# Kernel tuning notes

Hardware: AMD Instinct MI355X
Metric: run time of the kernel (lower is better)

## Reference

```python
import jax, jax.numpy as jnp
import numpy as np

EPS = 1e-12  # F.normalize eps
TEMP = 0.03


def _l2norm(x):
    # torch F.normalize: x / max(||x||, eps)
    n = jnp.sqrt(jnp.sum(x * x, axis=-1, keepdims=True))
    return x / jnp.maximum(n, EPS)


def setup_inputs() -> dict:
    key = jax.random.key(0)
    ks = jax.random.split(key, 8)
    B, C, H, W = 8, 256, 64, 64
    M = 2024
    Ch = C // 4
    s = 1.0 / np.sqrt(C)
    return {
        "feats": jax.random.normal(ks[0], (B, C, H, W), jnp.float32),
        "fg_memory": jax.random.normal(ks[1], (M, C), jnp.float32) * s,
        "bg_memory": jax.random.normal(ks[2], (M, C), jnp.float32) * s,
        "w1_fg": jax.random.normal(ks[3], (C, Ch), jnp.float32) * s,
        "b1_fg": jnp.zeros((Ch,), jnp.float32),
        "w2_fg": jax.random.normal(ks[4], (Ch, 1), jnp.float32) * (1.0 / np.sqrt(Ch)),
        "b2_fg": jnp.zeros((1,), jnp.float32),
        "w1_bg": jax.random.normal(ks[5], (C, Ch), jnp.float32) * s,
        "b1_bg": jnp.zeros((Ch,), jnp.float32),
        "w2_bg": jax.random.normal(ks[6], (Ch, 1), jnp.float32) * (1.0 / np.sqrt(Ch)),
        "b2_bg": jnp.zeros((1,), jnp.float32),
    }


def _gate(x, w1, b1, w2, b2):
    h = jax.nn.relu(x @ w1 + b1)
    return jax.nn.sigmoid(h @ w2 + b2)  # [N,1]


def reference(feats, fg_memory, bg_memory, w1_fg, b1_fg, w2_fg, b2_fg,
              w1_bg, b1_bg, w2_bg, b2_bg):
    B, C, H, W = feats.shape
    x = jnp.transpose(feats, (0, 2, 3, 1)).reshape(-1, C)  # [N,C]
    xn = _l2norm(x)
    fgn = _l2norm(fg_memory)  # [M,C]
    bgn = _l2norm(bg_memory)

    attn_fg = jax.nn.softmax((xn @ fgn.T) / TEMP, axis=1)  # [N,M]
    mem_fg = attn_fg @ fgn                                  # [N,C]
    attn_bg = jax.nn.softmax((xn @ bgn.T) / TEMP, axis=1)
    mem_bg = attn_bg @ bgn

    g_fg = _gate(xn, w1_fg, b1_fg, w2_fg, b2_fg)
    g_bg = _gate(xn, w1_bg, b1_bg, w2_bg, b2_bg)

    fused = xn + g_fg * mem_fg - g_bg * mem_bg
    return jnp.transpose(fused.reshape(B, H, W, C), (0, 3, 1, 2))
```

## Files before the change

kernel.cpp:

```cpp
#include <hip/hip_runtime.h>
#include <math.h>

#define B_   8
#define C_   256
#define HW_  4096
#define N_   32768
#define M_   2024
#define MP_  2048
#define CH_  64
#define NCHUNK (MP_ / 64)
#define INV_TEMP 33.333333333333336f
#define NEPS 1e-12f

typedef __attribute__((ext_vector_type(8))) short short8;
typedef __attribute__((ext_vector_type(4))) float floatx4;

__device__ __forceinline__ unsigned short f2bf(float f) {
  union { float f; unsigned u; } v; v.f = f;
  unsigned r = v.u + 0x7FFFu + ((v.u >> 16) & 1u);
  return (unsigned short)(r >> 16);
}
__device__ __forceinline__ float bf2f(unsigned short b) {
  union { unsigned u; float f; } v; v.u = ((unsigned)b) << 16; return v.f;
}

__device__ __forceinline__ void barrier_lds_only() {
  asm volatile("s_waitcnt lgkmcnt(0)\n\ts_barrier" ::: "memory");
}

__device__ __forceinline__ void async_copy16(const unsigned short* gsrc,
                                             unsigned short* lds) {
  __builtin_amdgcn_global_load_lds(
      (const __attribute__((address_space(1))) void*)gsrc,
      (__attribute__((address_space(3))) void*)lds, 16, 0, 0);
}

__global__ __launch_bounds__(256) void norm_mem_kernel(
    const float* __restrict__ fg, const float* __restrict__ bg,
    const float* __restrict__ w1f, const float* __restrict__ w1b,
    unsigned short* __restrict__ fgS, unsigned short* __restrict__ bgS,
    unsigned short* __restrict__ fgT, unsigned short* __restrict__ bgT) {
  __shared__ unsigned short tile[64][258];
  int bid = blockIdx.x;
  int t = threadIdx.x;
  int rr = t >> 2, c4 = t & 3;

  if (bid >= 64) {
    const float* srcw = (bid == 64) ? w1f : w1b;
    unsigned short* ms = (bid == 64) ? fgS : bgS;
#pragma unroll
    for (int i = 0; i < 16; ++i) {
      int c = c4 * 64 + i * 4;
      ushort4 o;
      o.x = f2bf(srcw[(size_t)(c + 0) * CH_ + rr]);
      o.y = f2bf(srcw[(size_t)(c + 1) * CH_ + rr]);
      o.z = f2bf(srcw[(size_t)(c + 2) * CH_ + rr]);
      o.w = f2bf(srcw[(size_t)(c + 3) * CH_ + rr]);
      int unit = (32 * 32 + (c >> 5) * 4 + ((c >> 3) & 3)) * 64 + rr;
      *(ushort4*)&ms[(size_t)unit * 8 + (c & 7)] = o;
    }
    return;
  }

  const float* src; unsigned short *ms, *mt; int r0;
  if (bid < 32) { src = fg; ms = fgS; mt = fgT; r0 = bid * 64; }
  else          { src = bg; ms = bgS; mt = bgT; r0 = (bid - 32) * 64; }
  int row = r0 + rr;
  int chunk = r0 >> 6;
  float v[64];
  float s = 0.f;
  if (row < M_) {
    const float4* p = (const float4*)(src + (size_t)row * C_ + c4 * 64);
#pragma unroll
    for (int i = 0; i < 16; ++i) {
      float4 q = p[i];
      v[i * 4 + 0] = q.x; v[i * 4 + 1] = q.y; v[i * 4 + 2] = q.z; v[i * 4 + 3] = q.w;
      s += q.x * q.x + q.y * q.y + q.z * q.z + q.w * q.w;
    }
  } else {
#pragma unroll
    for (int i = 0; i < 64; ++i) v[i] = 0.f;
  }
  s += __shfl_xor(s, 1, 64);
  s += __shfl_xor(s, 2, 64);
  float inv = (row < M_) ? 1.0f / fmaxf(sqrtf(s), NEPS) : 0.f;
#pragma unroll
  for (int i = 0; i < 16; ++i) {
    int c = c4 * 64 + i * 4;
    ushort4 o;
    o.x = f2bf(v[i * 4 + 0] * inv); o.y = f2bf(v[i * 4 + 1] * inv);
    o.z = f2bf(v[i * 4 + 2] * inv); o.w = f2bf(v[i * 4 + 3] * inv);
    int unit = (chunk * 32 + (c >> 5) * 4 + ((c >> 3) & 3)) * 64 + rr;
    *(ushort4*)&ms[(size_t)unit * 8 + (c & 7)] = o;
    *(ushort4*)&tile[rr][c] = o;
  }
  __syncthreads();
  int m = t & 63, cw = t >> 6;
#pragma unroll 8
  for (int j = 0; j < 64; ++j) {
    int c = cw * 64 + j;
    mt[(size_t)c * MP_ + r0 + m] = tile[m][c];
  }
}

__global__ __launch_bounds__(256) void prep_x_kernel(
    const float* __restrict__ feats, float* __restrict__ invn,
    unsigned short* __restrict__ xnb) {
  __shared__ unsigned short tileb[256][66];
  __shared__ float part[4][64];
  __shared__ float invs[64];
  int t = threadIdx.x, hwl = t & 63, cw = t >> 6;
  int n0 = blockIdx.x * 64;
  int b = n0 >> 12, hw0 = n0 & 4095;
  const float* p = feats + (size_t)b * C_ * HW_ + hw0 + hwl;
  float s = 0.f;
#pragma unroll 8
  for (int i = 0; i < 64; ++i) {
    int c = cw * 64 + i;
    float v = p[(size_t)c * HW_];
    s += v * v;
    tileb[c][hwl] = f2bf(v);
  }
  part[cw][hwl] = s;
  __syncthreads();
  if (t < 64) {
    float tot = part[0][t] + part[1][t] + part[2][t] + part[3][t];
    float inv = 1.0f / fmaxf(sqrtf(tot), NEPS);
    invn[n0 + t] = inv;
    invs[t] = inv;
  }
  __syncthreads();
  int px = t >> 2, q = t & 3;
  float iv = invs[px];
  unsigned short* xp = xnb + (size_t)(n0 + px) * C_;
#pragma unroll
  for (int blk = 0; blk < 8; ++blk) {
    int cb = blk * 4 + q;
    short8 o;
#pragma unroll
    for (int j = 0; j < 8; ++j)
      o[j] = (short)f2bf(bf2f(tileb[cb * 8 + j][px]) * iv);
    *(short8*)&xp[cb * 8] = o;
  }
}

__device__ __forceinline__ void stage_chunk(const unsigned short* memS, int mc,
                                            unsigned short* mtile, int w, int l) {
  const unsigned short* src = memS + (size_t)mc * 16384;
#pragma unroll
  for (int it = 0; it < 4; ++it) {
    int seg = (it * 8 + w) * 512;
    async_copy16(src + seg + l * 8, mtile + seg);
  }
}

__global__ __launch_bounds__(512, 4) void flash_fused_kernel(
    const unsigned short* __restrict__ xnb,
    const unsigned short* __restrict__ fgS, const unsigned short* __restrict__ fgT,
    const unsigned short* __restrict__ bgS, const unsigned short* __restrict__ bgT,
    const float* __restrict__ feats, const float* __restrict__ invn,
    const float* __restrict__ b1fp, const float* __restrict__ w2fp,
    const float* __restrict__ b2fp, const float* __restrict__ b1bp,
    const float* __restrict__ w2bp, const float* __restrict__ b2bp,
    float* __restrict__ out) {
  __shared__ __align__(16) char smem[49920];
  unsigned short* mtile = (unsigned short*)smem;
  unsigned short* Pbuf0 = (unsigned short*)(smem + 32768);
  unsigned short* Pbuf1 = (unsigned short*)(smem + 40960);
  float* rowsum = (float*)(smem + 49152);
  float* comb   = (float*)(smem + 49408);
  float* gpart  = (float*)(smem + 49664);
  float* trans  = (float*)smem;

  int t = threadIdx.x;
  int w = t >> 6, l = t & 63;
  int lm = l & 15, quad = l >> 4;
  int rg = w & 3, mh = w >> 2;
  int row0 = blockIdx.x * 64;

  short8 afrag[8];
  {
    const unsigned short* ap = xnb + (size_t)(row0 + 16 * rg + lm) * C_ + quad * 8;
#pragma unroll
    for (int kb = 0; kb < 8; ++kb)
      afrag[kb] = *(const short8*)(ap + kb * 32);
  }

  int bb = row0 >> 12, hw0 = row0 & 4095;
  float iv = invn[row0 + l];
  size_t ob = (size_t)bb * (size_t)C_ * HW_ + hw0 + l;

#pragma unroll 1
  for (int pass = 0; pass < 2; ++pass) {
    const unsigned short* memS  = pass ? bgS : fgS;
    const unsigned short* membT = pass ? bgT : fgT;

    floatx4 accO[4][2];
#pragma unroll
    for (int rt = 0; rt < 4; ++rt)
#pragma unroll
      for (int ct = 0; ct < 2; ++ct) accO[rt][ct] = (floatx4){0.f, 0.f, 0.f, 0.f};
    float rs[4] = {0.f, 0.f, 0.f, 0.f};
    if (t < 64) { rowsum[t] = 0.f; gpart[t] = 0.f; }

    stage_chunk(memS, 0, mtile, w, l);

#pragma unroll 1
    for (int mc = 0; mc < NCHUNK; ++mc) {
      __syncthreads();

      short8 bfT[2][2];
#pragma unroll
      for (int ct = 0; ct < 2; ++ct) {
        const unsigned short* tp =
            membT + (size_t)(w * 32 + ct * 16 + lm) * MP_ + mc * 64 + quad * 8;
        bfT[ct][0] = *(const short8*)(tp);
        bfT[ct][1] = *(const short8*)(tp + 32);
      }

      floatx4 accS[2];
      accS[0] = (floatx4){0.f, 0.f, 0.f, 0.f};
      accS[1] = (floatx4){0.f, 0.f, 0.f, 0.f};
#pragma unroll
      for (int mt2 = 0; mt2 < 2; ++mt2) {
        int mrow = mh * 32 + mt2 * 16 + lm;
#pragma unroll
        for (int kb = 0; kb < 8; ++kb) {
          short8 bf = *(const short8*)&mtile[(size_t)(((kb * 4 + quad) * 64) + mrow) * 8];
          accS[mt2] = __builtin_amdgcn_mfma_f32_16x16x32_bf16(afrag[kb], bf, accS[mt2], 0, 0, 0);
        }
      }

      unsigned short* P = (mc & 1) ? Pbuf1 : Pbuf0;
#pragma unroll
      for (int mt2 = 0; mt2 < 2; ++mt2) {
        int m = mh * 32 + mt2 * 16 + lm;
        float ebias = (mc * 64 + m < M_) ? 0.f : -1e30f;
        int g = mh * 4 + mt2 * 2 + (lm >> 3);
#pragma unroll
        for (int r = 0; r < 4; ++r) {
          float pv = __expf(__builtin_fmaf(accS[mt2][r], INV_TEMP, ebias));
          unsigned short pb = f2bf(pv);
          rs[r] += bf2f(pb);
          P[(g * 64 + 16 * rg + quad * 4 + r) * 8 + (lm & 7)] = pb;
        }
      }
      barrier_lds_only();

      stage_chunk(memS, mc + 1, mtile, w, l);

#pragma unroll
      for (int rt = 0; rt < 4; ++rt) {
        short8 pf0 = *(const short8*)&P[(size_t)((0 + quad) * 64 + rt * 16 + lm) * 8];
        short8 pf1 = *(const short8*)&P[(size_t)((4 + quad) * 64 + rt * 16 + lm) * 8];
#pragma unroll
        for (int ct = 0; ct < 2; ++ct) {
          accO[rt][ct] = __builtin_amdgcn_mfma_f32_16x16x32_bf16(pf0, bfT[ct][0], accO[rt][ct], 0, 0, 0);
          accO[rt][ct] = __builtin_amdgcn_mfma_f32_16x16x32_bf16(pf1, bfT[ct][1], accO[rt][ct], 0, 0, 0);
        }
      }
    }

    __syncthreads();
    {
      const float* b1p = pass ? b1bp : b1fp;
      const float* w2p = pass ? w2bp : w2fp;
      floatx4 accS[2];
      accS[0] = (floatx4){0.f, 0.f, 0.f, 0.f};
      accS[1] = (floatx4){0.f, 0.f, 0.f, 0.f};
#pragma unroll
      for (int mt2 = 0; mt2 < 2; ++mt2) {
        int mrow = mh * 32 + mt2 * 16 + lm;
#pragma unroll
        for (int kb = 0; kb < 8; ++kb) {
          short8 bf = *(const short8*)&mtile[(size_t)(((kb * 4 + quad) * 64) + mrow) * 8];
          accS[mt2] = __builtin_amdgcn_mfma_f32_16x16x32_bf16(afrag[kb], bf, accS[mt2], 0, 0, 0);
        }
      }
      float b1a = b1p[mh * 32 + lm];
      float b1c = b1p[mh * 32 + 16 + lm];
      float w2a = w2p[mh * 32 + lm];
      float w2c = w2p[mh * 32 + 16 + lm];
      float p[4];
#pragma unroll
      for (int r = 0; r < 4; ++r)
        p[r] = fmaxf(accS[0][r] + b1a, 0.f) * w2a +
               fmaxf(accS[1][r] + b1c, 0.f) * w2c;
#pragma unroll
      for (int off = 1; off < 16; off <<= 1)
#pragma unroll
        for (int r = 0; r < 4; ++r) p[r] += __shfl_xor(p[r], off, 64);
      if (lm == 0) {
#pragma unroll
        for (int r = 0; r < 4; ++r)
          atomicAdd(&gpart[16 * rg + quad * 4 + r], p[r]);
      }
    }

#pragma unroll
    for (int off = 1; off < 16; off <<= 1)
#pragma unroll
      for (int r = 0; r < 4; ++r) rs[r] += __shfl_xor(rs[r], off, 64);
    if (lm == 0) {
#pragma unroll
      for (int r = 0; r < 4; ++r) atomicAdd(&rowsum[16 * rg + quad * 4 + r], rs[r]);
    }
    __syncthreads();
    if (t < 64) {
      float b2v = (pass ? b2bp : b2fp)[0];
      float g = 1.f / (1.f + __expf(-(gpart[t] + b2v)));
      comb[t] = g / rowsum[t];
    }
    __syncthreads();

#pragma unroll 1
    for (int cg2 = 0; cg2 < 4; ++cg2) {
      if ((w >> 1) == cg2) {
#pragma unroll
        for (int rt = 0; rt < 4; ++rt)
#pragma unroll
          for (int r = 0; r < 4; ++r) {
            float cf = comb[16 * rt + quad * 4 + r];
#pragma unroll
            for (int ct = 0; ct < 2; ++ct)
              trans[(16 * rt + quad * 4 + r) * 67 + (w & 1) * 32 + ct * 16 + lm] =
                  cf * accO[rt][ct][r];
          }
      }
      __syncthreads();
      if (pass == 0) {
#pragma unroll
        for (int i = 0; i < 8; ++i) {
          int cl = w * 8 + i;
          int cg = cg2 * 64 + cl;
          out[ob + (size_t)cg * HW_] = trans[l * 67 + cl];
        }
      } else {
#pragma unroll
        for (int i = 0; i < 8; ++i) {
          int cl = w * 8 + i;
          int cg = cg2 * 64 + cl;
          size_t a = ob + (size_t)cg * HW_;
          out[a] = feats[a] * iv + out[a] - trans[l * 67 + cl];
        }
      }
      __syncthreads();
    }
  }
}

extern "C" void kernel_launch(void* const* d_in, const int* in_sizes, int n_in,
                              void* d_out, int out_size, void* d_ws, size_t ws_size,
                              hipStream_t stream) {
  const float* feats = (const float*)d_in[0];
  const float* fg    = (const float*)d_in[1];
  const float* bg    = (const float*)d_in[2];
  const float* w1f   = (const float*)d_in[3];
  const float* b1f   = (const float*)d_in[4];
  const float* w2f   = (const float*)d_in[5];
  const float* b2f   = (const float*)d_in[6];
  const float* w1b   = (const float*)d_in[7];
  const float* b1b   = (const float*)d_in[8];
  const float* w2b   = (const float*)d_in[9];
  const float* b2b   = (const float*)d_in[10];
  float* out = (float*)d_out;

  char* ws = (char*)d_ws;
  unsigned short* xnb = (unsigned short*)ws;
  unsigned short* fgS = xnb + (size_t)N_ * C_;
  unsigned short* bgS = fgS + (size_t)(MP_ + 64) * C_;
  unsigned short* fgT = bgS + (size_t)(MP_ + 64) * C_;
  unsigned short* bgT = fgT + (size_t)C_ * MP_;
  float* invn = (float*)(bgT + (size_t)C_ * MP_);

  norm_mem_kernel<<<66, 256, 0, stream>>>(fg, bg, w1f, w1b, fgS, bgS, fgT, bgT);
  prep_x_kernel<<<N_ / 64, 256, 0, stream>>>(feats, invn, xnb);
  flash_fused_kernel<<<N_ / 64, 512, 0, stream>>>(
      xnb, fgS, fgT, bgS, bgT, feats, invn,
      b1f, w2f, b2f, b1b, w2b, b2b, out);
}
```

Measured before the change: 305.9 us.

## Fuse input normalization into flash kernel, removing prep_x launch

Removes the separate prep_x kernel. The flash kernel now reads its 64 rows of feats directly, computes per-pixel L2 norms with a shared-memory reduction, writes normalized bf16 rows into a padded LDS tile and loads the MFMA A-fragments from it. This drops one launch and the global round trip of the bf16 normalized-x buffer and inverse-norm array. In exchange it adds extra syncthreads and 32 live floats per thread in the prologue, which may raise register pressure under launch_bounds(512,4).

```diff
diff --git a/kernel.cpp b/kernel.cpp
--- a/kernel.cpp
+++ b/kernel.cpp
@@ -103,47 +103,6 @@
   }
 }
 
-__global__ __launch_bounds__(256) void prep_x_kernel(
-    const float* __restrict__ feats, float* __restrict__ invn,
-    unsigned short* __restrict__ xnb) {
-  __shared__ unsigned short tileb[256][66];
-  __shared__ float part[4][64];
-  __shared__ float invs[64];
-  int t = threadIdx.x, hwl = t & 63, cw = t >> 6;
-  int n0 = blockIdx.x * 64;
-  int b = n0 >> 12, hw0 = n0 & 4095;
-  const float* p = feats + (size_t)b * C_ * HW_ + hw0 + hwl;
-  float s = 0.f;
-#pragma unroll 8
-  for (int i = 0; i < 64; ++i) {
-    int c = cw * 64 + i;
-    float v = p[(size_t)c * HW_];
-    s += v * v;
-    tileb[c][hwl] = f2bf(v);
-  }
-  part[cw][hwl] = s;
-  __syncthreads();
-  if (t < 64) {
-    float tot = part[0][t] + part[1][t] + part[2][t] + part[3][t];
-    float inv = 1.0f / fmaxf(sqrtf(tot), NEPS);
-    invn[n0 + t] = inv;
-    invs[t] = inv;
-  }
-  __syncthreads();
-  int px = t >> 2, q = t & 3;
-  float iv = invs[px];
-  unsigned short* xp = xnb + (size_t)(n0 + px) * C_;
-#pragma unroll
-  for (int blk = 0; blk < 8; ++blk) {
-    int cb = blk * 4 + q;
-    short8 o;
-#pragma unroll
-    for (int j = 0; j < 8; ++j)
-      o[j] = (short)f2bf(bf2f(tileb[cb * 8 + j][px]) * iv);
-    *(short8*)&xp[cb * 8] = o;
-  }
-}
-
 __device__ __forceinline__ void stage_chunk(const unsigned short* memS, int mc,
                                             unsigned short* mtile, int w, int l) {
   const unsigned short* src = memS + (size_t)mc * 16384;
@@ -155,10 +114,9 @@
 }
 
 __global__ __launch_bounds__(512, 4) void flash_fused_kernel(
-    const unsigned short* __restrict__ xnb,
     const unsigned short* __restrict__ fgS, const unsigned short* __restrict__ fgT,
     const unsigned short* __restrict__ bgS, const unsigned short* __restrict__ bgT,
-    const float* __restrict__ feats, const float* __restrict__ invn,
+    const float* __restrict__ feats,
     const float* __restrict__ b1fp, const float* __restrict__ w2fp,
     const float* __restrict__ b2fp, const float* __restrict__ b1bp,
     const float* __restrict__ w2bp, const float* __restrict__ b2bp,
@@ -171,24 +129,56 @@
   float* comb   = (float*)(smem + 49408);
   float* gpart  = (float*)(smem + 49664);
   float* trans  = (float*)smem;
+  unsigned short* xtile = (unsigned short*)smem;
+  float* part = (float*)(smem + 33792);
+  float* invs = (float*)(smem + 35840);
 
   int t = threadIdx.x;
   int w = t >> 6, l = t & 63;
   int lm = l & 15, quad = l >> 4;
   int rg = w & 3, mh = w >> 2;
   int row0 = blockIdx.x * 64;
-
+  int bb = row0 >> 12, hw0 = row0 & 4095;
+  size_t ob = (size_t)bb * (size_t)C_ * HW_ + hw0 + l;
+
+  float iv;
   short8 afrag[8];
   {
-    const unsigned short* ap = xnb + (size_t)(row0 + 16 * rg + lm) * C_ + quad * 8;
+    const float* p = feats + (size_t)bb * C_ * HW_ + hw0 + l;
+    float vv[32];
+    float s = 0.f;
+#pragma unroll
+    for (int i = 0; i < 32; ++i) {
+      float v = p[(size_t)(w * 32 + i) * HW_];
+      vv[i] = v;
+      s += v * v;
+    }
+    part[w * 64 + l] = s;
+    __syncthreads();
+    if (t < 64) {
+      float tot = 0.f;
+#pragma unroll
+      for (int j = 0; j < 8; ++j) tot += part[j * 64 + t];
+      invs[t] = 1.0f / fmaxf(sqrtf(tot), NEPS);
+    }
+    __syncthreads();
+    float ivl = invs[l];
+    unsigned short* xr = xtile + l * 264 + w * 32;
+#pragma unroll
+    for (int i = 0; i < 32; i += 8) {
+      short8 o;
+#pragma unroll
+      for (int j = 0; j < 8; ++j) o[j] = (short)f2bf(vv[i + j] * ivl);
+      *(short8*)&xr[i] = o;
+    }
+    __syncthreads();
+    iv = invs[l];
+    const unsigned short* xb = xtile + (16 * rg + lm) * 264 + quad * 8;
 #pragma unroll
     for (int kb = 0; kb < 8; ++kb)
-      afrag[kb] = *(const short8*)(ap + kb * 32);
-  }
-
-  int bb = row0 >> 12, hw0 = row0 & 4095;
-  float iv = invn[row0 + l];
-  size_t ob = (size_t)bb * (size_t)C_ * HW_ + hw0 + l;
+      afrag[kb] = *(const short8*)(xb + kb * 32);
+    __syncthreads();
+  }
 
 #pragma unroll 1
   for (int pass = 0; pass < 2; ++pass) {
@@ -366,16 +356,13 @@
   float* out = (float*)d_out;
 
   char* ws = (char*)d_ws;
-  unsigned short* xnb = (unsigned short*)ws;
-  unsigned short* fgS = xnb + (size_t)N_ * C_;
+  unsigned short* fgS = (unsigned short*)ws;
   unsigned short* bgS = fgS + (size_t)(MP_ + 64) * C_;
   unsigned short* fgT = bgS + (size_t)(MP_ + 64) * C_;
   unsigned short* bgT = fgT + (size_t)C_ * MP_;
-  float* invn = (float*)(bgT + (size_t)C_ * MP_);
 
   norm_mem_kernel<<<66, 256, 0, stream>>>(fg, bg, w1f, w1b, fgS, bgS, fgT, bgT);
-  prep_x_kernel<<<N_ / 64, 256, 0, stream>>>(feats, invn, xnb);
   flash_fused_kernel<<<N_ / 64, 512, 0, stream>>>(
-      xnb, fgS, fgT, bgS, bgT, feats, invn,
+      fgS, fgT, bgS, bgT, feats,
       b1f, w2f, b2f, b1b, w2b, b2b, out);
 }
```

Result: faster. 296.0 us (-3.2%).
